# Performance work log

Measured on AMD Instinct MI355X. Metric: run time of the kernel, lower is better.

The kernel has to match this reference:

```python
import jax, jax.numpy as jnp
import numpy as np

N = 50000       # nodes
E = 800000      # edges
F_IN = 197      # node_feature_dim
H = 256         # hidden_dim
HEADS = 8
HD = H // HEADS # 32
L = 5           # num_layers
FF = 4 * H      # 1024
C = 2           # num_classes
ED = 2          # edge_feature_dim
SCALE = float(np.sqrt(HD))


def _ln(x, g, b):
    m = x.mean(-1, keepdims=True)
    v = ((x - m) ** 2).mean(-1, keepdims=True)
    return (x - m) / jnp.sqrt(v + 1e-5) * g + b


def setup_inputs() -> dict:
    key = jax.random.key(0)
    ks = iter(jax.random.split(key, 40))
    d = {}
    d["x"] = jax.random.normal(next(ks), (N, F_IN), dtype=jnp.float32)
    d["edge_index"] = jax.random.randint(next(ks), (2, E), 0, N, dtype=jnp.int64)
    d["edge_attr"] = jax.random.normal(next(ks), (E, ED), dtype=jnp.float32)
    xav = lambda k, sh: jax.random.normal(k, sh, dtype=jnp.float32) * float(np.sqrt(2.0 / (sh[-2] + sh[-1])))
    # input projection + LN
    d["in_W"] = xav(next(ks), (F_IN, H)); d["in_b"] = jnp.zeros((H,), jnp.float32)
    d["in_g"] = jnp.ones((H,), jnp.float32); d["in_bb"] = jnp.zeros((H,), jnp.float32)
    # stacked per-layer params (leading dim L)
    d["Wq"] = xav(next(ks), (L, H, H)); d["Wk"] = xav(next(ks), (L, H, H)); d["Wv"] = xav(next(ks), (L, H, H))
    d["We"] = xav(next(ks), (L, ED, HEADS)); d["be"] = jnp.zeros((L, HEADS), jnp.float32)
    d["Wo"] = xav(next(ks), (L, H, H)); d["bo"] = jnp.zeros((L, H), jnp.float32)
    d["ln1_g"] = jnp.ones((L, H), jnp.float32); d["ln1_b"] = jnp.zeros((L, H), jnp.float32)
    d["ln2_g"] = jnp.ones((L, H), jnp.float32); d["ln2_b"] = jnp.zeros((L, H), jnp.float32)
    d["f1_W"] = xav(next(ks), (L, H, FF)); d["f1_b"] = jnp.zeros((L, FF), jnp.float32)
    d["f2_W"] = xav(next(ks), (L, FF, H)); d["f2_b"] = jnp.zeros((L, H), jnp.float32)
    # classifier
    d["cls1_W"] = xav(next(ks), (H, H // 2)); d["cls1_b"] = jnp.zeros((H // 2,), jnp.float32)
    d["cls2_W"] = xav(next(ks), (H // 2, C)); d["cls2_b"] = jnp.zeros((C,), jnp.float32)
    return d


def _forward(x, edge_index, edge_attr, in_W, in_b, in_g, in_bb,
             Wq, Wk, Wv, We, be, Wo, bo, ln1_g, ln1_b, ln2_g, ln2_b,
             f1_W, f1_b, f2_W, f2_b, cls1_W, cls1_b, cls2_W, cls2_b):
    src, dst = edge_index[0], edge_index[1]  # message flows src -> dst
    h = jax.nn.gelu(_ln(x @ in_W + in_b, in_g, in_bb), approximate=False)

    def layer(h, p):
        wq, wk, wv, we, b_e, wo, b_o, g1, b1, g2, b2, w1, bf1, w2, bf2 = p
        hn = _ln(h, g1, b1)
        q = (hn @ wq).reshape(-1, HEADS, HD)
        k = (hn @ wk).reshape(-1, HEADS, HD)
        v = (hn @ wv).reshape(-1, HEADS, HD)
        edge_bias = edge_attr @ we + b_e                        # (E, HEADS)
        score = (q[dst] * k[src]).sum(-1) / SCALE + edge_bias   # (E, HEADS)
        # segment softmax over destination nodes
        mx = jax.ops.segment_max(score, dst, num_segments=N)
        mx = jnp.where(jnp.isfinite(mx), mx, 0.0)
        ex = jnp.exp(score - mx[dst])
        denom = jax.ops.segment_sum(ex, dst, num_segments=N)
        w = ex / (denom[dst] + 1e-16)                           # (E, HEADS)
        msg = w[:, :, None] * v[src]                            # (E, HEADS, HD)
        agg = jax.ops.segment_sum(msg.reshape(-1, H), dst, num_segments=N)
        out = agg @ wo + b_o
        out = _ln(out + h, g2, b2)                              # residual_proj = Identity
        ffn = jax.nn.gelu(out @ w1 + bf1, approximate=False) @ w2 + bf2
        return out + ffn, None

    params = (Wq, Wk, Wv, We, be, Wo, bo, ln1_g, ln1_b, ln2_g, ln2_b, f1_W, f1_b, f2_W, f2_b)
    h, _ = jax.lax.scan(layer, h, params)
    logits = jax.nn.gelu(h @ cls1_W + cls1_b, approximate=False) @ cls2_W + cls2_b
    probs = jax.nn.softmax(logits, axis=-1)
    return logits, probs


def reference(x, edge_index, edge_attr, in_W, in_b, in_g, in_bb,
              Wq, Wk, Wv, We, be, Wo, bo, ln1_g, ln1_b, ln2_g, ln2_b,
              f1_W, f1_b, f2_W, f2_b, cls1_W, cls1_b, cls2_W, cls2_b):
    return _forward(x, edge_index, edge_attr, in_W, in_b, in_g, in_bb,
                    Wq, Wk, Wv, We, be, Wo, bo, ln1_g, ln1_b, ln2_g, ln2_b,
                    f1_W, f1_b, f2_W, f2_b, cls1_W, cls1_b, cls2_W, cls2_b)
```

## Files before the change

### kernel.cpp

```cpp
#include <hip/hip_runtime.h>
#include <math.h>

#define NN 50000
#define NE 800000
#define FIN 197
#define KIN 224
#define H 256
#define HEADS 8
#define HD 32
#define LAYERS 5
#define FF 1024
#define INV_SCALE 0.17677669529663687f

typedef __attribute__((ext_vector_type(8))) short short8;
typedef __attribute__((ext_vector_type(4))) float f32x4;
typedef unsigned short ushort;

__device__ __forceinline__ float gelu_f(float x) {
    float x2 = x * x;
    float u = __builtin_fmaf(0.044715f * x2, x, x);
    float e = __builtin_amdgcn_exp2f(-2.3022075f * u);
    return x * __builtin_amdgcn_rcpf(1.0f + e);
}
__device__ __forceinline__ ushort f2b(float f) {
    unsigned u = __float_as_uint(f);
    u += 0x7fffu + ((u >> 16) & 1u);
    return (ushort)(u >> 16);
}
__device__ __forceinline__ float b2f(ushort b) {
    return __uint_as_float(((unsigned)b) << 16);
}
__device__ __forceinline__ float dot2b(unsigned a, unsigned b) {
    float a0 = __uint_as_float(a << 16), a1 = __uint_as_float(a & 0xffff0000u);
    float b0 = __uint_as_float(b << 16), b1 = __uint_as_float(b & 0xffff0000u);
    return a0 * b0 + a1 * b1;
}

__device__ __forceinline__ void load16_lds(const ushort* gp, ushort* lp) {
    __builtin_amdgcn_global_load_lds(
        (const __attribute__((address_space(1))) unsigned int*)gp,
        (__attribute__((address_space(3))) unsigned int*)lp,
        16, 0, 0);
}

__global__ __launch_bounds__(256) void gemm_bf16_kernel(
    const ushort* __restrict__ A, int lda,
    const ushort* __restrict__ Bt,
    const float* __restrict__ bias,
    const float* __restrict__ res, int ldr,
    float* __restrict__ Cf, ushort* __restrict__ Cb, int ldc,
    int n, int K, int act, int gx)
{
    __shared__ ushort As[2][128 * 32];
    __shared__ ushort Bs[2][128 * 32];
    int tid = threadIdx.x;
    int lane = tid & 63;
    int wave = tid >> 6;

    int tiles_y = (n + 127) >> 7;
    int lin = blockIdx.x;
    int gsz = gx * 8;
    int group = lin / gsz;
    int rem = lin - group * gsz;
    int rows_left = tiles_y - group * 8;
    int rg = rows_left < 8 ? rows_left : 8;
    int r = rem % rg;
    int c = rem / rg;
    int brow = (group * 8 + r) * 128;
    int bcol = c * 128;

    f32x4 acc[2][8] = {};
    int m0 = lane & 15;
    int rdc = ((lane >> 4) ^ ((lane >> 1) & 3)) * 8;

    int rA = lane >> 2;
    int c8s = (((lane & 3) ^ ((lane >> 3) & 3)) * 8);

    long arow0, arow1, brow0, brow1;
    {
        int gr0 = brow + wave * 32 + rA;        if (gr0 >= n) gr0 = n - 1;
        int gr1 = brow + wave * 32 + 16 + rA;   if (gr1 >= n) gr1 = n - 1;
        arow0 = (long)gr0 * lda;
        arow1 = (long)gr1 * lda;
        brow0 = (long)(bcol + wave * 32 + rA) * K;
        brow1 = (long)(bcol + wave * 32 + 16 + rA) * K;
    }
    int lo0 = (wave * 32) * 32;
    int lo1 = (wave * 32 + 16) * 32;

    int nt = K >> 5;
    load16_lds(A + arow0 + c8s, &As[0][lo0]);
    load16_lds(A + arow1 + c8s, &As[0][lo1]);
    load16_lds(Bt + brow0 + c8s, &Bs[0][lo0]);
    load16_lds(Bt + brow1 + c8s, &Bs[0][lo1]);
    __syncthreads();

    for (int t = 0; t < nt; ++t) {
        int p = t & 1;
        if (t + 1 < nt) {
            int k0 = (t + 1) << 5;
            load16_lds(A + arow0 + k0 + c8s, &As[p ^ 1][lo0]);
            load16_lds(A + arow1 + k0 + c8s, &As[p ^ 1][lo1]);
            load16_lds(Bt + brow0 + k0 + c8s, &Bs[p ^ 1][lo0]);
            load16_lds(Bt + brow1 + k0 + c8s, &Bs[p ^ 1][lo1]);
        }
        short8 af[2], bfr[8];
        #pragma unroll
        for (int i = 0; i < 2; ++i)
            af[i] = *(const short8*)&As[p][(wave * 32 + i * 16 + m0) * 32 + rdc];
        #pragma unroll
        for (int j = 0; j < 8; ++j)
            bfr[j] = *(const short8*)&Bs[p][(j * 16 + m0) * 32 + rdc];
        #pragma unroll
        for (int i = 0; i < 2; ++i)
            #pragma unroll
            for (int j = 0; j < 8; ++j)
                acc[i][j] = __builtin_amdgcn_mfma_f32_16x16x32_bf16(af[i], bfr[j], acc[i][j], 0, 0, 0);
        __syncthreads();
    }

    float* ch0 = (float*)&As[0][wave * 1024];
    float* ch1 = (float*)&As[1][wave * 1024];
    float* ch2 = (float*)&Bs[0][wave * 1024];
    float* ch3 = (float*)&Bs[1][wave * 1024];
    int ccol = lane & 15;
    int mych = lane >> 4;
    float* wch = (mych == 0) ? ch0 : ((mych == 1) ? ch1 : ((mych == 2) ? ch2 : ch3));
    int gcol = bcol + (lane & 31) * 4;
    #pragma unroll
    for (int i = 0; i < 2; ++i) {
        int rowbase = brow + wave * 32 + i * 16;
        #pragma unroll
        for (int rr = 0; rr < 4; ++rr)
            #pragma unroll
            for (int j = 0; j < 8; ++j)
                wch[rr * 128 + j * 16 + ccol] = acc[i][j][rr];
        #pragma unroll
        for (int k = 0; k < 8; ++k) {
            const float* rch = ((k >> 1) == 0) ? ch0 :
                               (((k >> 1) == 1) ? ch1 :
                               (((k >> 1) == 2) ? ch2 : ch3));
            f32x4 v = *(const f32x4*)&rch[(((k & 1) * 64) + lane) * 4];
            int grow = rowbase + 2 * k + (lane >> 5);
            if (bias) {
                float4 b4 = *(const float4*)(bias + gcol);
                v[0] += b4.x; v[1] += b4.y; v[2] += b4.z; v[3] += b4.w;
            }
            if (act) {
                v[0] = gelu_f(v[0]); v[1] = gelu_f(v[1]);
                v[2] = gelu_f(v[2]); v[3] = gelu_f(v[3]);
            }
            if (grow < n) {
                if (res) {
                    float4 r4 = *(const float4*)(res + (long)grow * ldr + gcol);
                    v[0] += r4.x; v[1] += r4.y; v[2] += r4.z; v[3] += r4.w;
                }
                if (Cf) *(f32x4*)(Cf + (long)grow * ldc + gcol) = v;
                if (Cb) {
                    ushort4 ob = { f2b(v[0]), f2b(v[1]), f2b(v[2]), f2b(v[3]) };
                    *(ushort4*)(Cb + (long)grow * ldc + gcol) = ob;
                }
            }
        }
        if (i == 0) __syncthreads();
    }
}

__global__ __launch_bounds__(256) void ln256_kernel(
    const float* __restrict__ af, const ushort* __restrict__ ab,
    const float* __restrict__ res,
    const float* __restrict__ g, const float* __restrict__ bta,
    float* __restrict__ outf, ushort* __restrict__ outb, int n, int post_gelu)
{
    int row = blockIdx.x * 4 + (threadIdx.x >> 6);
    if (row >= n) return;
    int lane = threadIdx.x & 63;
    float4 v;
    if (af) {
        v = *(const float4*)(af + (long)row * H + lane * 4);
    } else {
        ushort4 vb = *(const ushort4*)(ab + (long)row * H + lane * 4);
        v.x = b2f(vb.x); v.y = b2f(vb.y); v.z = b2f(vb.z); v.w = b2f(vb.w);
    }
    if (res) {
        float4 r = *(const float4*)(res + (long)row * H + lane * 4);
        v.x += r.x; v.y += r.y; v.z += r.z; v.w += r.w;
    }
    float s = v.x + v.y + v.z + v.w;
    #pragma unroll
    for (int off = 1; off < 64; off <<= 1) s += __shfl_xor(s, off);
    float mean = s * (1.0f / H);
    float dx = v.x - mean, dy = v.y - mean, dz = v.z - mean, dw = v.w - mean;
    float qs = dx * dx + dy * dy + dz * dz + dw * dw;
    #pragma unroll
    for (int off = 1; off < 64; off <<= 1) qs += __shfl_xor(qs, off);
    float rstd = rsqrtf(qs * (1.0f / H) + 1e-5f);
    float4 gg = *(const float4*)(g + lane * 4);
    float4 bb = *(const float4*)(bta + lane * 4);
    float4 o;
    o.x = dx * rstd * gg.x + bb.x;
    o.y = dy * rstd * gg.y + bb.y;
    o.z = dz * rstd * gg.z + bb.z;
    o.w = dw * rstd * gg.w + bb.w;
    if (post_gelu) { o.x = gelu_f(o.x); o.y = gelu_f(o.y); o.z = gelu_f(o.z); o.w = gelu_f(o.w); }
    if (outf) *(float4*)(outf + (long)row * H + lane * 4) = o;
    if (outb) {
        ushort4 ob = { f2b(o.x), f2b(o.y), f2b(o.z), f2b(o.w) };
        *(ushort4*)(outb + (long)row * H + lane * 4) = ob;
    }
}

__global__ __launch_bounds__(256) void xcast_kernel(const float* __restrict__ x,
                                                    ushort* __restrict__ xb)
{
    long i = (long)blockIdx.x * 256 + threadIdx.x;
    if (i >= (long)NN * KIN) return;
    int n = (int)(i / KIN), c = (int)(i % KIN);
    xb[i] = (c < FIN) ? f2b(x[(long)n * FIN + c]) : (ushort)0;
}

__global__ __launch_bounds__(256) void wtin_kernel(const float* __restrict__ W,
                                                   ushort* __restrict__ Wt)
{
    int i = blockIdx.x * 256 + threadIdx.x;
    if (i >= 256 * KIN) return;
    int m = i / KIN, k = i % KIN;
    Wt[i] = (k < FIN) ? f2b(W[(long)k * H + m]) : (ushort)0;
}

__global__ __launch_bounds__(256) void wtqkv_kernel(
    const float* __restrict__ Wq, const float* __restrict__ Wk,
    const float* __restrict__ Wv, ushort* __restrict__ out)
{
    long i = (long)blockIdx.x * 256 + threadIdx.x;
    if (i >= (long)LAYERS * 768 * 256) return;
    int l = (int)(i / (768 * 256));
    int r = (int)(i % (768 * 256));
    int m = r >> 8, k = r & 255;
    const float* W = (m < 256) ? Wq : ((m < 512) ? Wk : Wv);
    out[i] = f2b(W[(long)l * 65536 + (long)k * 256 + (m & 255)]);
}

__global__ __launch_bounds__(256) void wtgen_kernel(
    const float* __restrict__ W, ushort* __restrict__ out, int L, int K, int M)
{
    long i = (long)blockIdx.x * 256 + threadIdx.x;
    if (i >= (long)L * K * M) return;
    int l = (int)(i / ((long)K * M));
    int r = (int)(i % ((long)K * M));
    int m = r / K, k = r % K;
    out[i] = f2b(W[(long)l * K * M + (long)k * M + m]);
}

__global__ __launch_bounds__(256) void deg_kernel(const int* __restrict__ dst,
                                                   int* __restrict__ deg)
{
    int e = blockIdx.x * 256 + threadIdx.x;
    if (e >= NE) return;
    atomicAdd(&deg[dst[e]], 1);
}

__global__ __launch_bounds__(256) void scan1_kernel(const int* __restrict__ deg,
                                                     int* __restrict__ rowptr,
                                                     int* __restrict__ bsum)
{
    __shared__ int buf[256];
    int tid = threadIdx.x;
    int i = blockIdx.x * 256 + tid;
    int v = (i < NN) ? deg[i] : 0;
    buf[tid] = v;
    __syncthreads();
    #pragma unroll
    for (int off = 1; off < 256; off <<= 1) {
        int t = (tid >= off) ? buf[tid - off] : 0;
        __syncthreads();
        buf[tid] += t;
        __syncthreads();
    }
    if (i < NN) rowptr[i] = buf[tid] - v;
    if (tid == 255) bsum[blockIdx.x] = buf[255];
}

__global__ __launch_bounds__(256) void scan2_kernel(int* __restrict__ bsum, int nb)
{
    __shared__ int buf[256];
    int tid = threadIdx.x;
    int v = (tid < nb) ? bsum[tid] : 0;
    buf[tid] = v;
    __syncthreads();
    #pragma unroll
    for (int off = 1; off < 256; off <<= 1) {
        int t = (tid >= off) ? buf[tid - off] : 0;
        __syncthreads();
        buf[tid] += t;
        __syncthreads();
    }
    if (tid < nb) bsum[tid] = buf[tid] - v;
}

__global__ __launch_bounds__(256) void scan3_kernel(int* __restrict__ rowptr,
                                                     const int* __restrict__ bsum)
{
    int i = blockIdx.x * 256 + threadIdx.x;
    if (i < NN) rowptr[i] += bsum[blockIdx.x];
    if (i == 0) rowptr[NN] = NE;
}

__global__ __launch_bounds__(256) void fill_kernel(
    const int* __restrict__ src, const int* __restrict__ dst,
    const float* __restrict__ ea, const int* __restrict__ rowptr,
    int* __restrict__ cursor, int* __restrict__ csr_src,
    float2* __restrict__ csr_ea)
{
    int e = blockIdx.x * 256 + threadIdx.x;
    if (e >= NE) return;
    int d = dst[e];
    int pos = atomicAdd(&cursor[d], 1);
    int j = rowptr[d] + pos;
    csr_src[j] = src[e];
    csr_ea[j] = *(const float2*)(ea + 2 * e);
}

#define LOADE(idx, kbuf, vbuf, ebuf)                                   \
    { int s_ = csr_src[idx]; ebuf = csr_ea[idx];                       \
      const ushort* kr_ = qkv + (long)s_ * 768 + 256;                  \
      kbuf = *(const uint2*)(kr_ + lane * 4);                          \
      vbuf = *(const uint2*)(kr_ + 256 + lane * 4); }

#define PAIR(k1, v1, e1, k2, v2, e2)                                               \
    { float p1 = dot2b(q2.x, (k1).x) + dot2b(q2.y, (k1).y);                        \
      float p2 = dot2b(q2.x, (k2).x) + dot2b(q2.y, (k2).y);                        \
      p1 += __shfl_xor(p1, 1);  p2 += __shfl_xor(p2, 1);                           \
      p1 += __shfl_xor(p1, 2);  p2 += __shfl_xor(p2, 2);                           \
      p1 += __shfl_xor(p1, 4);  p2 += __shfl_xor(p2, 4);                           \
      float s1 = p1 * c1 + (e1).x * w0 + (e1).y * w1 + bb;                         \
      float s2 = p2 * c1 + (e2).x * w0 + (e2).y * w1 + bb;                         \
      float mp = fmaxf(s1, s2);                                                    \
      float x1 = __builtin_amdgcn_exp2f(s1 - mp);                                  \
      float x2 = __builtin_amdgcn_exp2f(s2 - mp);                                  \
      float lp = x1 + x2;                                                          \
      float b0 = x1 * __uint_as_float((v1).x << 16)         + x2 * __uint_as_float((v2).x << 16);          \
      float b1 = x1 * __uint_as_float((v1).x & 0xffff0000u) + x2 * __uint_as_float((v2).x & 0xffff0000u);  \
      float b2 = x1 * __uint_as_float((v1).y << 16)         + x2 * __uint_as_float((v2).y << 16);          \
      float b3 = x1 * __uint_as_float((v1).y & 0xffff0000u) + x2 * __uint_as_float((v2).y & 0xffff0000u);  \
      float mn = fmaxf(m, mp);                                                     \
      float so = __builtin_amdgcn_exp2f(m - mn);                                   \
      float sp = __builtin_amdgcn_exp2f(mp - mn);                                  \
      l  = l  * so + lp * sp;                                                      \
      a0 = a0 * so + b0 * sp;                                                      \
      a1 = a1 * so + b1 * sp;                                                      \
      a2 = a2 * so + b2 * sp;                                                      \
      a3 = a3 * so + b3 * sp;                                                      \
      m = mn; }

#define SINGLE(kb, vb, eb)                                                         \
    { float p1 = dot2b(q2.x, (kb).x) + dot2b(q2.y, (kb).y);                        \
      p1 += __shfl_xor(p1, 1);                                                     \
      p1 += __shfl_xor(p1, 2);                                                     \
      p1 += __shfl_xor(p1, 4);                                                     \
      float s1 = p1 * c1 + (eb).x * w0 + (eb).y * w1 + bb;                         \
      float mn = fmaxf(m, s1);                                                     \
      float so = __builtin_amdgcn_exp2f(m - mn);                                   \
      float e_ = __builtin_amdgcn_exp2f(s1 - mn);                                  \
      l  = l  * so + e_;                                                           \
      a0 = a0 * so + e_ * __uint_as_float((vb).x << 16);                           \
      a1 = a1 * so + e_ * __uint_as_float((vb).x & 0xffff0000u);                   \
      a2 = a2 * so + e_ * __uint_as_float((vb).y << 16);                           \
      a3 = a3 * so + e_ * __uint_as_float((vb).y & 0xffff0000u);                   \
      m = mn; }

__global__ __launch_bounds__(256) void attn_kernel(
    const ushort* __restrict__ qkv,
    const int* __restrict__ rowptr, const int* __restrict__ csr_src,
    const float2* __restrict__ csr_ea,
    const float* __restrict__ We, const float* __restrict__ be,
    ushort* __restrict__ aggb)
{
    int node = blockIdx.x * 4 + (threadIdx.x >> 6);
    if (node >= NN) return;
    int lane = threadIdx.x & 63;
    int h = lane >> 3;
    const float L2E = 1.4426950408889634f;
    float w0 = We[h] * L2E, w1 = We[8 + h] * L2E, bb = be[h] * L2E;
    const float c1 = INV_SCALE * L2E;

    uint2 q2 = *(const uint2*)(qkv + (long)node * 768 + lane * 4);
    int jbeg = rowptr[node], jend = rowptr[node + 1];

    float m = -1e30f, l = 0.f;
    float a0 = 0.f, a1 = 0.f, a2 = 0.f, a3 = 0.f;

    uint2 k0v = {0,0}, v0v = {0,0}, k1v = {0,0}, v1v = {0,0};
    uint2 k2v = {0,0}, v2v = {0,0}, k3v = {0,0}, v3v = {0,0};
    float2 e0v = {0.f,0.f}, e1v = {0.f,0.f}, e2v = {0.f,0.f}, e3v = {0.f,0.f};

    if (jbeg + 0 < jend) LOADE(jbeg + 0, k0v, v0v, e0v);
    if (jbeg + 1 < jend) LOADE(jbeg + 1, k1v, v1v, e1v);
    if (jbeg + 2 < jend) LOADE(jbeg + 2, k2v, v2v, e2v);
    if (jbeg + 3 < jend) LOADE(jbeg + 3, k3v, v3v, e3v);

    int j = jbeg;
    for (; j + 3 < jend; j += 4) {
        PAIR(k0v, v0v, e0v, k1v, v1v, e1v);
        if (j + 4 < jend) LOADE(j + 4, k0v, v0v, e0v);
        if (j + 5 < jend) LOADE(j + 5, k1v, v1v, e1v);
        PAIR(k2v, v2v, e2v, k3v, v3v, e3v);
        if (j + 6 < jend) LOADE(j + 6, k2v, v2v, e2v);
        if (j + 7 < jend) LOADE(j + 7, k3v, v3v, e3v);
    }
    int rleft = jend - j;
    if (rleft >= 2) PAIR(k0v, v0v, e0v, k1v, v1v, e1v);
    if (rleft == 3) SINGLE(k2v, v2v, e2v);
    if (rleft == 1) SINGLE(k0v, v0v, e0v);

    float inv = 1.0f / (l + 1e-16f);
    ushort4 o = { f2b(a0 * inv), f2b(a1 * inv), f2b(a2 * inv), f2b(a3 * inv) };
    *(ushort4*)(aggb + (long)node * 256 + lane * 4) = o;
}

__global__ __launch_bounds__(256) void cls_kernel(
    const float* __restrict__ t1, const float* __restrict__ W,
    const float* __restrict__ b, float* __restrict__ out)
{
    int i = blockIdx.x * 256 + threadIdx.x;
    if (i >= NN) return;
    const float* tp = t1 + (long)i * 128;
    float a0 = 0.f, a1 = 0.f;
    #pragma unroll
    for (int j = 0; j < 128; j += 4) {
        float4 t = *(const float4*)(tp + j);
        a0 += t.x * W[(j + 0) * 2] + t.y * W[(j + 1) * 2] + t.z * W[(j + 2) * 2] + t.w * W[(j + 3) * 2];
        a1 += t.x * W[(j + 0) * 2 + 1] + t.y * W[(j + 1) * 2 + 1] + t.z * W[(j + 2) * 2 + 1] + t.w * W[(j + 3) * 2 + 1];
    }
    float l0 = a0 + b[0], l1 = a1 + b[1];
    out[(long)i * 2 + 0] = l0;
    out[(long)i * 2 + 1] = l1;
    float mx = fmaxf(l0, l1);
    float p0 = expf(l0 - mx), p1 = expf(l1 - mx);
    float sden = p0 + p1;
    out[2L * NN + (long)i * 2 + 0] = p0 / sden;
    out[2L * NN + (long)i * 2 + 1] = p1 / sden;
}

extern "C" void kernel_launch(void* const* d_in, const int* in_sizes, int n_in,
                              void* d_out, int out_size, void* d_ws, size_t ws_size,
                              hipStream_t stream) {
    const float* x      = (const float*)d_in[0];
    const int*   ei     = (const int*)d_in[1];
    const float* ea     = (const float*)d_in[2];
    const float* in_W   = (const float*)d_in[3];
    const float* in_b   = (const float*)d_in[4];
    const float* in_g   = (const float*)d_in[5];
    const float* in_bb  = (const float*)d_in[6];
    const float* Wq     = (const float*)d_in[7];
    const float* Wk     = (const float*)d_in[8];
    const float* Wv     = (const float*)d_in[9];
    const float* We     = (const float*)d_in[10];
    const float* be     = (const float*)d_in[11];
    const float* Wo     = (const float*)d_in[12];
    const float* bo     = (const float*)d_in[13];
    const float* ln1_g  = (const float*)d_in[14];
    const float* ln1_b  = (const float*)d_in[15];
    const float* ln2_g  = (const float*)d_in[16];
    const float* ln2_b  = (const float*)d_in[17];
    const float* f1_W   = (const float*)d_in[18];
    const float* f1_b   = (const float*)d_in[19];
    const float* f2_W   = (const float*)d_in[20];
    const float* f2_b   = (const float*)d_in[21];
    const float* cls1_W = (const float*)d_in[22];
    const float* cls1_b = (const float*)d_in[23];
    const float* cls2_W = (const float*)d_in[24];
    const float* cls2_b = (const float*)d_in[25];
    float* out = (float*)d_out;

    const int* src = ei;
    const int* dst = ei + NE;

    char* w = (char*)d_ws;
    float* B0 = (float*)w;            w += (size_t)NN * H * 4;
    ushort* hb = (ushort*)w;          w += (size_t)NN * H * 2;
    char* pool = w;                   w += (size_t)NN * 1024 * 2;
    ushort* qkv  = (ushort*)pool;
    ushort* aggb = (ushort*)(pool + (size_t)NN * 768 * 2);
    float*  tproj = (float*)pool;
    ushort* xb   = (ushort*)(pool + (size_t)NN * H * 4);
    ushort* tb   = (ushort*)pool;
    float*  t1   = (float*)pool;
    int* deg    = (int*)w;            w += (size_t)NN * 4;
    int* cursor = (int*)w;            w += (size_t)NN * 4;
    int* rowptr = (int*)w;            w += (size_t)(NN + 2) * 4;
    int* bsum   = (int*)w;            w += 1024;
    int* csr_src = (int*)w;           w += (size_t)NE * 4;
    float2* csr_ea = (float2*)w;      w += (size_t)NE * 8;
    ushort* wqkv_t = (ushort*)w;      w += (size_t)LAYERS * 768 * 256 * 2;
    ushort* wo_t  = (ushort*)w;       w += (size_t)LAYERS * 65536 * 2;
    ushort* f1_t  = (ushort*)w;       w += (size_t)LAYERS * 262144 * 2;
    ushort* f2_t  = (ushort*)w;       w += (size_t)LAYERS * 262144 * 2;
    ushort* c1_t  = (ushort*)w;       w += (size_t)32768 * 2;
    ushort* inw_t = (ushort*)w;       w += (size_t)256 * KIN * 2;

    dim3 blk(256);
    const int ln_grid = (NN + 3) / 4;
    const int e_grid = (NE + 255) / 256;
    const int n_grid = (NN + 255) / 256;
    const int ty = (NN + 127) / 128;

    hipMemsetAsync(deg, 0, (size_t)NN * 4, stream);
    hipMemsetAsync(cursor, 0, (size_t)NN * 4, stream);
    deg_kernel<<<e_grid, blk, 0, stream>>>(dst, deg);
    scan1_kernel<<<n_grid, blk, 0, stream>>>(deg, rowptr, bsum);
    scan2_kernel<<<1, blk, 0, stream>>>(bsum, n_grid);
    scan3_kernel<<<n_grid, blk, 0, stream>>>(rowptr, bsum);
    fill_kernel<<<e_grid, blk, 0, stream>>>(src, dst, ea, rowptr, cursor, csr_src, csr_ea);

    wtqkv_kernel<<<(int)(((long)LAYERS * 768 * 256 + 255) / 256), blk, 0, stream>>>(Wq, Wk, Wv, wqkv_t);
    wtgen_kernel<<<(int)(((long)LAYERS * 65536 + 255) / 256), blk, 0, stream>>>(Wo, wo_t, LAYERS, 256, 256);
    wtgen_kernel<<<(int)(((long)LAYERS * 262144 + 255) / 256), blk, 0, stream>>>(f1_W, f1_t, LAYERS, 256, 1024);
    wtgen_kernel<<<(int)(((long)LAYERS * 262144 + 255) / 256), blk, 0, stream>>>(f2_W, f2_t, LAYERS, 1024, 256);
    wtgen_kernel<<<(32768 + 255) / 256, blk, 0, stream>>>(cls1_W, c1_t, 1, 256, 128);
    wtin_kernel<<<(256 * KIN + 255) / 256, blk, 0, stream>>>(in_W, inw_t);

    xcast_kernel<<<(int)(((long)NN * KIN + 255) / 256), blk, 0, stream>>>(x, xb);
    {
        gemm_bf16_kernel<<<2 * ty, blk, 0, stream>>>(xb, KIN, inw_t, in_b, nullptr, 0,
                                                     tproj, nullptr, H, NN, KIN, 0, 2);
        ln256_kernel<<<ln_grid, blk, 0, stream>>>(tproj, nullptr, nullptr, in_g, in_bb, B0, nullptr, NN, 1);
    }

    for (int l = 0; l < LAYERS; ++l) {
        const float* we  = We + (long)l * 16;
        const float* bel = be + (long)l * 8;
        const float* bol = bo + (long)l * H;
        const float* g1 = ln1_g + (long)l * H;
        const float* b1 = ln1_b + (long)l * H;
        const float* g2 = ln2_g + (long)l * H;
        const float* b2 = ln2_b + (long)l * H;
        const float* bf1 = f1_b + (long)l * FF;
        const float* bf2 = f2_b + (long)l * H;

        ln256_kernel<<<ln_grid, blk, 0, stream>>>(B0, nullptr, nullptr, g1, b1, nullptr, hb, NN, 0);

        gemm_bf16_kernel<<<6 * ty, blk, 0, stream>>>(hb, H, wqkv_t + (long)l * 768 * 256,
            nullptr, nullptr, 0, nullptr, qkv, 768, NN, H, 0, 6);
        attn_kernel<<<(NN + 3) / 4, blk, 0, stream>>>(qkv, rowptr, csr_src, csr_ea, we, bel, aggb);

        gemm_bf16_kernel<<<2 * ty, blk, 0, stream>>>(aggb, H, wo_t + (long)l * 65536,
            bol, nullptr, 0, nullptr, qkv, H, NN, H, 0, 2);
        ln256_kernel<<<ln_grid, blk, 0, stream>>>(nullptr, qkv, B0, g2, b2, B0, hb, NN, 0);

        gemm_bf16_kernel<<<8 * ty, blk, 0, stream>>>(hb, H, f1_t + (long)l * 262144,
            bf1, nullptr, 0, nullptr, tb, FF, NN, H, 1, 8);
        gemm_bf16_kernel<<<2 * ty, blk, 0, stream>>>(tb, FF, f2_t + (long)l * 262144,
            bf2, B0, H, B0, (l == LAYERS - 1) ? hb : nullptr, H, NN, FF, 0, 2);
    }

    {
        gemm_bf16_kernel<<<1 * ty, blk, 0, stream>>>(hb, H, c1_t, cls1_b, nullptr, 0,
                                                     t1, nullptr, 128, NN, H, 1, 1);
        cls_kernel<<<n_grid, blk, 0, stream>>>(t1, cls2_W, cls2_b, out);
    }
}
```

Baseline: 2.074 ms.

## Fuse output-projection and FFN2 GEMMs with residual add and LayerNorm

Adds a GEMM kernel in which each block computes 64 full rows of the 256-wide output, so the bias, the residual from B0 and a full-row LayerNorm can be applied in registers. The Wo GEMM now fuses the LN2 step, and the FFN2 GEMM fuses the residual and the next layer's LN1 (the first LN1 is hoisted before the loop). This removes two standalone LayerNorm passes and their global round trips per layer. The trade-off is a large accumulator footprint per wave and narrower per-lane epilogue stores. It also drops a __syncthreads from the existing GEMM epilogue, which could race if shared staging is reused.

```diff
diff --git a/kernel.cpp b/kernel.cpp
--- a/kernel.cpp
+++ b/kernel.cpp
@@ -162,7 +162,137 @@
                 }
             }
         }
-        if (i == 0) __syncthreads();
+    }
+}
+
+__global__ __launch_bounds__(256) void gemm_ln_kernel(
+    const ushort* __restrict__ A, int K,
+    const ushort* __restrict__ Bt,
+    const float* __restrict__ bias,
+    float* __restrict__ B0,
+    const float* __restrict__ g, const float* __restrict__ bta,
+    ushort* __restrict__ hb, int n,
+    int do_ln, int ln_to_b0, int write_b0)
+{
+    __shared__ ushort As[2][64 * 32];
+    __shared__ ushort Bs[2][256 * 32];
+    int tid = threadIdx.x;
+    int lane = tid & 63;
+    int wave = tid >> 6;
+    int brow = blockIdx.x * 64;
+    int wrow = brow + wave * 16;
+
+    f32x4 acc[16] = {};
+    int m0 = lane & 15;
+    int rdc = ((lane >> 4) ^ ((lane >> 1) & 3)) * 8;
+    int rA = lane >> 2;
+    int c8s = (((lane & 3) ^ ((lane >> 3) & 3)) * 8);
+
+    long arow;
+    { int gr = wrow + rA; if (gr >= n) gr = n - 1; arow = (long)gr * K; }
+    long brow0 = (long)(wave * 64 + rA) * K;
+    int loA = (wave * 16) * 32;
+    int loB = (wave * 64) * 32;
+
+    int nt = K >> 5;
+    load16_lds(A + arow + c8s, &As[0][loA]);
+    #pragma unroll
+    for (int q = 0; q < 4; ++q)
+        load16_lds(Bt + brow0 + (long)q * 16 * K + c8s, &Bs[0][loB + q * 16 * 32]);
+    __syncthreads();
+
+    for (int t = 0; t < nt; ++t) {
+        int p = t & 1;
+        if (t + 1 < nt) {
+            int k0 = (t + 1) << 5;
+            load16_lds(A + arow + k0 + c8s, &As[p ^ 1][loA]);
+            #pragma unroll
+            for (int q = 0; q < 4; ++q)
+                load16_lds(Bt + brow0 + (long)q * 16 * K + k0 + c8s,
+                           &Bs[p ^ 1][loB + q * 16 * 32]);
+        }
+        short8 af = *(const short8*)&As[p][(wave * 16 + m0) * 32 + rdc];
+        #pragma unroll
+        for (int jg = 0; jg < 4; ++jg) {
+            short8 b0r = *(const short8*)&Bs[p][((jg * 64) + m0) * 32 + rdc];
+            short8 b1r = *(const short8*)&Bs[p][((jg * 64) + 16 + m0) * 32 + rdc];
+            short8 b2r = *(const short8*)&Bs[p][((jg * 64) + 32 + m0) * 32 + rdc];
+            short8 b3r = *(const short8*)&Bs[p][((jg * 64) + 48 + m0) * 32 + rdc];
+            acc[jg * 4 + 0] = __builtin_amdgcn_mfma_f32_16x16x32_bf16(af, b0r, acc[jg * 4 + 0], 0, 0, 0);
+            acc[jg * 4 + 1] = __builtin_amdgcn_mfma_f32_16x16x32_bf16(af, b1r, acc[jg * 4 + 1], 0, 0, 0);
+            acc[jg * 4 + 2] = __builtin_amdgcn_mfma_f32_16x16x32_bf16(af, b2r, acc[jg * 4 + 2], 0, 0, 0);
+            acc[jg * 4 + 3] = __builtin_amdgcn_mfma_f32_16x16x32_bf16(af, b3r, acc[jg * 4 + 3], 0, 0, 0);
+        }
+        __syncthreads();
+    }
+
+    int li = lane & 15, lg = lane >> 4;
+    #pragma unroll
+    for (int j = 0; j < 16; ++j) {
+        float bj = bias[j * 16 + li];
+        #pragma unroll
+        for (int rr = 0; rr < 4; ++rr) {
+            int grow = wrow + lg * 4 + rr;
+            float rv = (grow < n) ? B0[(long)grow * H + j * 16 + li] : 0.f;
+            acc[j][rr] += bj + rv;
+        }
+    }
+    if (do_ln) {
+        float s0 = 0.f, s1 = 0.f, s2 = 0.f, s3 = 0.f;
+        #pragma unroll
+        for (int j = 0; j < 16; ++j) { s0 += acc[j][0]; s1 += acc[j][1]; s2 += acc[j][2]; s3 += acc[j][3]; }
+        #pragma unroll
+        for (int off = 1; off < 16; off <<= 1) {
+            s0 += __shfl_xor(s0, off); s1 += __shfl_xor(s1, off);
+            s2 += __shfl_xor(s2, off); s3 += __shfl_xor(s3, off);
+        }
+        float mn0 = s0 * (1.0f / H), mn1 = s1 * (1.0f / H), mn2 = s2 * (1.0f / H), mn3 = s3 * (1.0f / H);
+        float q0 = 0.f, q1 = 0.f, q2 = 0.f, q3 = 0.f;
+        #pragma unroll
+        for (int j = 0; j < 16; ++j) {
+            float d0 = acc[j][0] - mn0, d1 = acc[j][1] - mn1;
+            float d2 = acc[j][2] - mn2, d3 = acc[j][3] - mn3;
+            q0 += d0 * d0; q1 += d1 * d1; q2 += d2 * d2; q3 += d3 * d3;
+        }
+        #pragma unroll
+        for (int off = 1; off < 16; off <<= 1) {
+            q0 += __shfl_xor(q0, off); q1 += __shfl_xor(q1, off);
+            q2 += __shfl_xor(q2, off); q3 += __shfl_xor(q3, off);
+        }
+        float rs0 = rsqrtf(q0 * (1.0f / H) + 1e-5f);
+        float rs1 = rsqrtf(q1 * (1.0f / H) + 1e-5f);
+        float rs2 = rsqrtf(q2 * (1.0f / H) + 1e-5f);
+        float rs3 = rsqrtf(q3 * (1.0f / H) + 1e-5f);
+        #pragma unroll
+        for (int j = 0; j < 16; ++j) {
+            int col = j * 16 + li;
+            float gj = g[col], bj = bta[col];
+            float o0 = (acc[j][0] - mn0) * rs0 * gj + bj;
+            float o1 = (acc[j][1] - mn1) * rs1 * gj + bj;
+            float o2 = (acc[j][2] - mn2) * rs2 * gj + bj;
+            float o3 = (acc[j][3] - mn3) * rs3 * gj + bj;
+            #pragma unroll
+            for (int rr = 0; rr < 4; ++rr) {
+                int grow = wrow + lg * 4 + rr;
+                if (grow >= n) continue;
+                float ov = (rr == 0) ? o0 : ((rr == 1) ? o1 : ((rr == 2) ? o2 : o3));
+                if (write_b0)
+                    B0[(long)grow * H + col] = ln_to_b0 ? ov : acc[j][rr];
+                hb[(long)grow * H + col] = f2b(ov);
+            }
+        }
+    } else {
+        #pragma unroll
+        for (int j = 0; j < 16; ++j) {
+            int col = j * 16 + li;
+            #pragma unroll
+            for (int rr = 0; rr < 4; ++rr) {
+                int grow = wrow + lg * 4 + rr;
+                if (grow >= n) continue;
+                if (write_b0) B0[(long)grow * H + col] = acc[j][rr];
+                hb[(long)grow * H + col] = f2b(acc[j][rr]);
+            }
+        }
     }
 }
 
@@ -504,6 +634,7 @@
     const int e_grid = (NE + 255) / 256;
     const int n_grid = (NN + 255) / 256;
     const int ty = (NN + 127) / 128;
+    const int ty2 = (NN + 63) / 64;
 
     hipMemsetAsync(deg, 0, (size_t)NN * 4, stream);
     hipMemsetAsync(cursor, 0, (size_t)NN * 4, stream);
@@ -527,31 +658,35 @@
         ln256_kernel<<<ln_grid, blk, 0, stream>>>(tproj, nullptr, nullptr, in_g, in_bb, B0, nullptr, NN, 1);
     }
 
+    ln256_kernel<<<ln_grid, blk, 0, stream>>>(B0, nullptr, nullptr, ln1_g, ln1_b, nullptr, hb, NN, 0);
+
     for (int l = 0; l < LAYERS; ++l) {
         const float* we  = We + (long)l * 16;
         const float* bel = be + (long)l * 8;
         const float* bol = bo + (long)l * H;
-        const float* g1 = ln1_g + (long)l * H;
-        const float* b1 = ln1_b + (long)l * H;
         const float* g2 = ln2_g + (long)l * H;
         const float* b2 = ln2_b + (long)l * H;
         const float* bf1 = f1_b + (long)l * FF;
         const float* bf2 = f2_b + (long)l * H;
 
-        ln256_kernel<<<ln_grid, blk, 0, stream>>>(B0, nullptr, nullptr, g1, b1, nullptr, hb, NN, 0);
-
         gemm_bf16_kernel<<<6 * ty, blk, 0, stream>>>(hb, H, wqkv_t + (long)l * 768 * 256,
             nullptr, nullptr, 0, nullptr, qkv, 768, NN, H, 0, 6);
         attn_kernel<<<(NN + 3) / 4, blk, 0, stream>>>(qkv, rowptr, csr_src, csr_ea, we, bel, aggb);
 
-        gemm_bf16_kernel<<<2 * ty, blk, 0, stream>>>(aggb, H, wo_t + (long)l * 65536,
-            bol, nullptr, 0, nullptr, qkv, H, NN, H, 0, 2);
-        ln256_kernel<<<ln_grid, blk, 0, stream>>>(nullptr, qkv, B0, g2, b2, B0, hb, NN, 0);
+        gemm_ln_kernel<<<ty2, blk, 0, stream>>>(aggb, H, wo_t + (long)l * 65536,
+            bol, B0, g2, b2, hb, NN, 1, 1, 1);
 
         gemm_bf16_kernel<<<8 * ty, blk, 0, stream>>>(hb, H, f1_t + (long)l * 262144,
             bf1, nullptr, 0, nullptr, tb, FF, NN, H, 1, 8);
-        gemm_bf16_kernel<<<2 * ty, blk, 0, stream>>>(tb, FF, f2_t + (long)l * 262144,
-            bf2, B0, H, B0, (l == LAYERS - 1) ? hb : nullptr, H, NN, FF, 0, 2);
+
+        if (l + 1 < LAYERS) {
+            gemm_ln_kernel<<<ty2, blk, 0, stream>>>(tb, FF, f2_t + (long)l * 262144,
+                bf2, B0, ln1_g + (long)(l + 1) * H, ln1_b + (long)(l + 1) * H,
+                hb, NN, 1, 0, 1);
+        } else {
+            gemm_ln_kernel<<<ty2, blk, 0, stream>>>(tb, FF, f2_t + (long)l * 262144,
+                bf2, B0, nullptr, nullptr, hb, NN, 0, 0, 0);
+        }
     }
 
     {
```

After: 2.222 ms. +7.1%, slower.
